# Kernel tuning notes

Hardware: AMD Instinct MI355X
Metric: run time of the kernel (lower is better)

Reference implementation:

```python
import jax, jax.numpy as jnp
import numpy as np
import math

B, S, IN_DIM, OUT_DIM = 16, 1024, 512, 256
THETA = 10000.0


def _rope_single(x, cos, sin):
    # x: [B,S,D]; cos/sin: [D//2] -- SAME rotation applied at every position
    # (faithful to original: freqs_cis[seq_len*2] selects a single row)
    xr = x.reshape(x.shape[0], x.shape[1], -1, 2)
    a, b = xr[..., 0], xr[..., 1]
    out = jnp.stack([a * cos - b * sin, a * sin + b * cos], axis=-1)
    return out.reshape(x.shape)


def setup_inputs() -> dict:
    key = jax.random.key(0)
    ks = jax.random.split(key, 4)
    scale = 1.0 / math.sqrt(IN_DIM)
    x = jax.random.normal(ks[0], (B, S, IN_DIM), jnp.float32)
    wq = jax.random.normal(ks[1], (OUT_DIM, IN_DIM), jnp.float32) * scale
    wk = jax.random.normal(ks[2], (OUT_DIM, IN_DIM), jnp.float32) * scale
    wv = jax.random.normal(ks[3], (OUT_DIM, IN_DIM), jnp.float32) * scale
    bq = jnp.zeros((OUT_DIM,), jnp.float32)
    bk = jnp.zeros((OUT_DIM,), jnp.float32)
    bv = jnp.zeros((OUT_DIM,), jnp.float32)
    return {"x": x, "wq": wq, "bq": bq, "wk": wk, "bk": bk, "wv": wv, "bv": bv}


def reference(x, wq, bq, wk, bk, wv, bv):
    dim = x.shape[-1]  # scale uses INPUT dim, per original code
    # freqs_cis row at position index = 2*seq_len
    inv_freq = 1.0 / (THETA ** (jnp.arange(0, OUT_DIM, 2, dtype=jnp.float32) / OUT_DIM))
    angle = (2.0 * S) * inv_freq  # [OUT_DIM//2]
    cos, sin = jnp.cos(angle), jnp.sin(angle)

    q = jnp.einsum('bsi,oi->bso', x, wq) + bq
    k = jnp.einsum('bsi,oi->bso', x, wk) + bk
    v = jnp.einsum('bsi,oi->bso', x, wv) + bv

    q = _rope_single(q, cos, sin)
    k = _rope_single(k, cos, sin)

    scores = jnp.einsum('bqd,bkd->bqk', q, k) / jnp.sqrt(jnp.float32(dim))
    scores = jax.nn.softmax(scores.astype(jnp.float32), axis=-1)
    out = jnp.einsum('bqk,bkd->bqd', scores, v)
    return out
```

## Files before the change

kernel.cpp:

```cpp
#include <hip/hip_runtime.h>
#include <hip/hip_bf16.h>


typedef __attribute__((ext_vector_type(8))) short short8;
typedef __attribute__((ext_vector_type(4))) short short4v;
typedef __attribute__((ext_vector_type(4))) float f32x4;

#define GLL16(g, l)                                                            \
  __builtin_amdgcn_global_load_lds(                                            \
      (const __attribute__((address_space(1))) unsigned int*)(g),              \
      (__attribute__((address_space(3))) unsigned int*)(l), 16, 0, 0)

static __device__ __forceinline__ short f2bf(float f) {
  __hip_bfloat16 h = __float2bfloat16(f);
  return __builtin_bit_cast(short, h);
}

__global__ void cvt_w(const float* __restrict__ wq, const float* __restrict__ wk,
                      const float* __restrict__ wv, short* __restrict__ dst) {
  int i = blockIdx.x * blockDim.x + threadIdx.x;
  if (i >= 49152) return;
  const float* src;
  int off;
  if (i < 16384)      { src = wq; off = i; }
  else if (i < 32768) { src = wk; off = i - 16384; }
  else                { src = wv; off = i - 32768; }
  const float4* sp = reinterpret_cast<const float4*>(src) + off * 2;
  float4 a = sp[0], b = sp[1];
  short8 o;
  o[0] = f2bf(a.x); o[1] = f2bf(a.y); o[2] = f2bf(a.z); o[3] = f2bf(a.w);
  o[4] = f2bf(b.x); o[5] = f2bf(b.y); o[6] = f2bf(b.z); o[7] = f2bf(b.w);
  *(reinterpret_cast<short8*>(dst) + i) = o;
}

__global__ __launch_bounds__(256) void qkv_gemm(
    const float* __restrict__ x, const short* __restrict__ wb,
    const float* __restrict__ bq, const float* __restrict__ bk,
    const float* __restrict__ bv, short* __restrict__ qb,
    short* __restrict__ kb, short* __restrict__ vt) {
  __shared__ __align__(16) char smem[32768];
  const int bid = blockIdx.x;
  const int swz = (bid & 7) * 96 + (bid >> 3);
  const int mt = swz / 6, nt = swz % 6;
  const int tid = threadIdx.x;
  const int w = tid >> 6, lane = tid & 63;
  const int g = lane >> 4, c = lane & 15;
  const int wm = w >> 1, wn = w & 1;

  f32x4 acc[4][4];
  const f32x4 fzero = {0.f, 0.f, 0.f, 0.f};
#pragma unroll
  for (int mi = 0; mi < 4; mi++)
#pragma unroll
    for (int ni = 0; ni < 4; ni++) acc[mi][ni] = fzero;

  const int arow = tid >> 4;
  const int acol4 = tid & 15;
  const int achunk = acol4 >> 1, ahalf = (tid & 1) * 8;

  for (int kk = 0; kk < 8; ++kk) {
    __syncthreads();
#pragma unroll
    for (int i = 0; i < 4; i++) {
      int idx = w * 4 + i;
      int r = idx * 8 + (lane >> 3);
      int cc = lane & 7;
      GLL16(wb + (nt * 128 + r) * 512 + kk * 64 + ((cc ^ (r & 7)) * 8),
            smem + 16384 + idx * 1024);
    }
    float4 xv[8];
#pragma unroll
    for (int j = 0; j < 8; j++) {
      int row = j * 16 + arow;
      xv[j] = *(const float4*)(x + (mt * 128 + row) * 512 + kk * 64 + acol4 * 4);
    }
#pragma unroll
    for (int j = 0; j < 8; j++) {
      int row = j * 16 + arow;
      short4v s4;
      s4[0] = f2bf(xv[j].x); s4[1] = f2bf(xv[j].y);
      s4[2] = f2bf(xv[j].z); s4[3] = f2bf(xv[j].w);
      *(short4v*)(smem + row * 128 + ((achunk ^ (row & 7)) * 16) + ahalf) = s4;
    }
    asm volatile("s_waitcnt vmcnt(0)" ::: "memory");
    __syncthreads();
#pragma unroll
    for (int ks = 0; ks < 2; ++ks) {
      short8 af[4], bf[4];
#pragma unroll
      for (int mi = 0; mi < 4; mi++) {
        int row = wm * 64 + mi * 16 + c;
        af[mi] = *(const short8*)(smem + row * 128 + (((ks * 4 + g) ^ (row & 7)) * 16));
      }
#pragma unroll
      for (int ni = 0; ni < 4; ni++) {
        int row = wn * 64 + ni * 16 + c;
        bf[ni] = *(const short8*)(smem + 16384 + row * 128 + (((ks * 4 + g) ^ (row & 7)) * 16));
      }
#pragma unroll
      for (int mi = 0; mi < 4; mi++)
#pragma unroll
        for (int ni = 0; ni < 4; ni++)
          acc[mi][ni] = __builtin_amdgcn_mfma_f32_16x16x32_bf16(af[mi], bf[ni], acc[mi][ni], 0, 0, 0);
    }
  }

  const int colbase = nt * 128 + wn * 64;
  const int cls = colbase >> 8;
  const int cw = colbase & 255;
  const int rowbase = mt * 128 + wm * 64;
  if (cls == 0) {
#pragma unroll
    for (int ni = 0; ni < 4; ni++) {
      int col = cw + ni * 16 + c;
      float bias = bq[col];
#pragma unroll
      for (int mi = 0; mi < 4; mi++)
#pragma unroll
        for (int j = 0; j < 4; j++) {
          int row = rowbase + mi * 16 + g * 4 + j;
          qb[row * 256 + col] = f2bf((acc[mi][ni][j] + bias) * 0.044194173824159216f);
        }
    }
  } else if (cls == 1) {
#pragma unroll
    for (int ni = 0; ni < 4; ni++) {
      int col = cw + ni * 16 + c;
      float bias = bk[col];
#pragma unroll
      for (int mi = 0; mi < 4; mi++)
#pragma unroll
        for (int j = 0; j < 4; j++) {
          int row = rowbase + mi * 16 + g * 4 + j;
          kb[row * 256 + col] = f2bf(acc[mi][ni][j] + bias);
        }
    }
  } else {
    __syncthreads();
    char* tb = smem + w * 8192;
#pragma unroll
    for (int ni = 0; ni < 4; ni++) {
      int dl = ni * 16 + c;
      float bias = bv[cw + dl];
#pragma unroll
      for (int mi = 0; mi < 4; mi++)
#pragma unroll
        for (int j = 0; j < 4; j++) {
          int sl = mi * 16 + g * 4 + j;
          *(short*)(tb + dl * 128 + ((sl * 2) ^ ((dl & 7) << 4))) =
              f2bf(acc[mi][ni][j] + bias);
        }
    }
    const int bb = rowbase >> 10, sb = rowbase & 1023;
#pragma unroll
    for (int i = 0; i < 8; i++) {
      int dl = i * 8 + (lane >> 3);
      int ch = lane & 7;
      short8 val = *(const short8*)(tb + dl * 128 + (((ch ^ (dl & 7)) * 16)));
      *(short8*)(vt + (bb * 256 + cw + dl) * 1024 + sb + ch * 8) = val;
    }
  }
}

__global__ __launch_bounds__(256) void attn_kernel(
    const short* __restrict__ qb, const short* __restrict__ kb,
    const short* __restrict__ vt, float* __restrict__ out) {
  __shared__ __align__(16) char smem[140288];
  const int bid = blockIdx.x;
  const int swz = (bid & 7) * 32 + (bid >> 3);
  const int b = swz >> 4, qt = swz & 15;
  const int tid = threadIdx.x;
  const int w = tid >> 6, lane = tid & 63;
  const int g = lane >> 4, c = lane & 15;
  const int q0 = b * 1024 + qt * 64 + w * 16;
  const int VB = 65536, PB = 131072;
  short* sp = (short*)(smem + PB + w * 2304);

  short8 qf[8];
#pragma unroll
  for (int ks = 0; ks < 8; ks++)
    qf[ks] = *(const short8*)(qb + (q0 + c) * 256 + ks * 32 + g * 8);

  f32x4 O[16];
  const f32x4 fzero = {0.f, 0.f, 0.f, 0.f};
#pragma unroll
  for (int ni = 0; ni < 16; ni++) O[ni] = fzero;
  float m_[4] = {-1e30f, -1e30f, -1e30f, -1e30f};
  float l_[4] = {0.f, 0.f, 0.f, 0.f};

  auto stage = [&](int kt, int bsel) {
    if (w < 2) {
#pragma unroll
      for (int i = 0; i < 16; i++) {
        int j = w * 16 + i;
        int r = j * 2 + (lane >> 5);
        int cc = lane & 31;
        GLL16(kb + (b * 1024 + kt * 64 + r) * 256 + ((cc ^ (r & 7)) * 8),
              smem + bsel * 32768 + j * 1024);
      }
    } else {
#pragma unroll
      for (int i = 0; i < 16; i++) {
        int j = (w - 2) * 16 + i;
        int r = j * 8 + (lane >> 3);
        int cc = lane & 7;
        GLL16(vt + (b * 256 + r) * 1024 + kt * 64 + ((cc ^ (r & 7)) * 8),
              smem + VB + bsel * 32768 + j * 1024);
      }
    }
  };

  stage(0, 0);
  for (int kt = 0; kt < 16; ++kt) {
    const int cur = kt & 1;
    const char* kbase = smem + cur * 32768;
    const char* vbase = smem + VB + cur * 32768;
    asm volatile("s_waitcnt vmcnt(0)" ::: "memory");
    __syncthreads();
    if (kt < 15) stage(kt + 1, cur ^ 1);

    f32x4 Sf[4];
#pragma unroll
    for (int nf = 0; nf < 4; nf++) Sf[nf] = fzero;
#pragma unroll
    for (int ks = 0; ks < 8; ks++) {
      short8 kf[4];
#pragma unroll
      for (int nf = 0; nf < 4; nf++) {
        int key = nf * 16 + c;
        kf[nf] = *(const short8*)(kbase + key * 512 + (((ks * 4 + g) ^ (c & 7)) * 16));
      }
#pragma unroll
      for (int nf = 0; nf < 4; nf++)
        Sf[nf] = __builtin_amdgcn_mfma_f32_16x16x32_bf16(qf[ks], kf[nf], Sf[nf], 0, 0, 0);
    }

    float Pv[4][4], scl[4];
#pragma unroll
    for (int j = 0; j < 4; j++) {
      float tm = fmaxf(fmaxf(Sf[0][j], Sf[1][j]), fmaxf(Sf[2][j], Sf[3][j]));
      tm = fmaxf(tm, __shfl_xor(tm, 1));
      tm = fmaxf(tm, __shfl_xor(tm, 2));
      tm = fmaxf(tm, __shfl_xor(tm, 4));
      tm = fmaxf(tm, __shfl_xor(tm, 8));
      float nm = fmaxf(m_[j], tm);
      scl[j] = __expf(m_[j] - nm);
      m_[j] = nm;
      float rs = 0.f;
#pragma unroll
      for (int nf = 0; nf < 4; nf++) {
        float p = __expf(Sf[nf][j] - nm);
        Pv[nf][j] = p;
        rs += p;
      }
      rs += __shfl_xor(rs, 1);
      rs += __shfl_xor(rs, 2);
      rs += __shfl_xor(rs, 4);
      rs += __shfl_xor(rs, 8);
      l_[j] = l_[j] * scl[j] + rs;
    }
#pragma unroll
    for (int ni = 0; ni < 16; ni++) {
      O[ni][0] *= scl[0]; O[ni][1] *= scl[1];
      O[ni][2] *= scl[2]; O[ni][3] *= scl[3];
    }

#pragma unroll
    for (int nf = 0; nf < 4; nf++)
#pragma unroll
      for (int j = 0; j < 4; j++)
        sp[(g * 4 + j) * 72 + nf * 16 + c] = f2bf(Pv[nf][j]);

    short8 pf[2];
#pragma unroll
    for (int ks2 = 0; ks2 < 2; ks2++)
      pf[ks2] = *(const short8*)((char*)sp + c * 144 + ks2 * 64 + g * 16);

#pragma unroll
    for (int ni = 0; ni < 16; ni++) {
      int d = ni * 16 + c;
#pragma unroll
      for (int ks2 = 0; ks2 < 2; ks2++) {
        short8 vf = *(const short8*)(vbase + d * 128 + (((ks2 * 4 + g) ^ (c & 7)) * 16));
        O[ni] = __builtin_amdgcn_mfma_f32_16x16x32_bf16(pf[ks2], vf, O[ni], 0, 0, 0);
      }
    }
  }

#pragma unroll
  for (int j = 0; j < 4; j++) {
    float inv = 1.0f / l_[j];
    int row = q0 + g * 4 + j;
#pragma unroll
    for (int ni = 0; ni < 16; ni++)
      out[row * 256 + ni * 16 + c] = O[ni][j] * inv;
  }
}

extern "C" void kernel_launch(void* const* d_in, const int* in_sizes, int n_in,
                              void* d_out, int out_size, void* d_ws, size_t ws_size,
                              hipStream_t stream) {
  const float* x  = (const float*)d_in[0];
  const float* wq = (const float*)d_in[1];
  const float* bq = (const float*)d_in[2];
  const float* wk = (const float*)d_in[3];
  const float* bk = (const float*)d_in[4];
  const float* wv = (const float*)d_in[5];
  const float* bv = (const float*)d_in[6];
  float* out = (float*)d_out;
  char* ws = (char*)d_ws;
  short* wb = (short*)ws;
  short* qb = (short*)(ws + 786432);
  short* kb = (short*)(ws + 9175040);
  short* vt = (short*)(ws + 17563648);

  cvt_w<<<192, 256, 0, stream>>>(wq, wk, wv, wb);
  qkv_gemm<<<768, 256, 0, stream>>>(x, wb, bq, bk, bv, qb, kb, vt);
  attn_kernel<<<256, 256, 0, stream>>>(qb, kb, vt, out);
}
```

Before: 167.0 us.

## Fuse weight conversion into QKV GEMM and split attention keys across two wave groups

Drops the separate weight-conversion kernel. The QKV GEMM now loads fp32 weights directly and converts them to bf16 while staging them into shared memory, which removes one launch and the extra weight round trip. The attention kernel moves to 512 threads: two groups of four waves each process half of the key sequence, and their partial softmax states are merged through shared memory at the end (split-K flash attention). The key/value double-buffer prefetch is dropped in favour of synchronous loads per tile, so load latency may be less hidden, and the larger block may lower occupancy.

```diff
diff --git a/kernel.cpp b/kernel.cpp
--- a/kernel.cpp
+++ b/kernel.cpp
@@ -16,25 +16,9 @@
   return __builtin_bit_cast(short, h);
 }
 
-__global__ void cvt_w(const float* __restrict__ wq, const float* __restrict__ wk,
-                      const float* __restrict__ wv, short* __restrict__ dst) {
-  int i = blockIdx.x * blockDim.x + threadIdx.x;
-  if (i >= 49152) return;
-  const float* src;
-  int off;
-  if (i < 16384)      { src = wq; off = i; }
-  else if (i < 32768) { src = wk; off = i - 16384; }
-  else                { src = wv; off = i - 32768; }
-  const float4* sp = reinterpret_cast<const float4*>(src) + off * 2;
-  float4 a = sp[0], b = sp[1];
-  short8 o;
-  o[0] = f2bf(a.x); o[1] = f2bf(a.y); o[2] = f2bf(a.z); o[3] = f2bf(a.w);
-  o[4] = f2bf(b.x); o[5] = f2bf(b.y); o[6] = f2bf(b.z); o[7] = f2bf(b.w);
-  *(reinterpret_cast<short8*>(dst) + i) = o;
-}
-
 __global__ __launch_bounds__(256) void qkv_gemm(
-    const float* __restrict__ x, const short* __restrict__ wb,
+    const float* __restrict__ x, const float* __restrict__ wq,
+    const float* __restrict__ wk, const float* __restrict__ wv,
     const float* __restrict__ bq, const float* __restrict__ bk,
     const float* __restrict__ bv, short* __restrict__ qb,
     short* __restrict__ kb, short* __restrict__ vt) {
@@ -47,6 +31,9 @@
   const int g = lane >> 4, c = lane & 15;
   const int wm = w >> 1, wn = w & 1;
 
+  const float* wsel = (nt < 2) ? wq : (nt < 4) ? wk : wv;
+  const int wro = (nt & 1) * 128;
+
   f32x4 acc[4][4];
   const f32x4 fzero = {0.f, 0.f, 0.f, 0.f};
 #pragma unroll
@@ -60,19 +47,16 @@
 
   for (int kk = 0; kk < 8; ++kk) {
     __syncthreads();
-#pragma unroll
-    for (int i = 0; i < 4; i++) {
-      int idx = w * 4 + i;
-      int r = idx * 8 + (lane >> 3);
-      int cc = lane & 7;
-      GLL16(wb + (nt * 128 + r) * 512 + kk * 64 + ((cc ^ (r & 7)) * 8),
-            smem + 16384 + idx * 1024);
-    }
-    float4 xv[8];
+    float4 xv[8], wv8[8];
 #pragma unroll
     for (int j = 0; j < 8; j++) {
       int row = j * 16 + arow;
       xv[j] = *(const float4*)(x + (mt * 128 + row) * 512 + kk * 64 + acol4 * 4);
+    }
+#pragma unroll
+    for (int j = 0; j < 8; j++) {
+      int row = j * 16 + arow;
+      wv8[j] = *(const float4*)(wsel + (wro + row) * 512 + kk * 64 + acol4 * 4);
     }
 #pragma unroll
     for (int j = 0; j < 8; j++) {
@@ -81,8 +65,11 @@
       s4[0] = f2bf(xv[j].x); s4[1] = f2bf(xv[j].y);
       s4[2] = f2bf(xv[j].z); s4[3] = f2bf(xv[j].w);
       *(short4v*)(smem + row * 128 + ((achunk ^ (row & 7)) * 16) + ahalf) = s4;
-    }
-    asm volatile("s_waitcnt vmcnt(0)" ::: "memory");
+      short4v t4;
+      t4[0] = f2bf(wv8[j].x); t4[1] = f2bf(wv8[j].y);
+      t4[2] = f2bf(wv8[j].z); t4[3] = f2bf(wv8[j].w);
+      *(short4v*)(smem + 16384 + row * 128 + ((achunk ^ (row & 7)) * 16) + ahalf) = t4;
+    }
     __syncthreads();
 #pragma unroll
     for (int ks = 0; ks < 2; ++ks) {
@@ -105,9 +92,8 @@
     }
   }
 
-  const int colbase = nt * 128 + wn * 64;
-  const int cls = colbase >> 8;
-  const int cw = colbase & 255;
+  const int cls = nt >> 1;
+  const int cw = (nt & 1) * 128 + wn * 64;
   const int rowbase = mt * 128 + wm * 64;
   if (cls == 0) {
 #pragma unroll
@@ -156,25 +142,27 @@
     for (int i = 0; i < 8; i++) {
       int dl = i * 8 + (lane >> 3);
       int ch = lane & 7;
-      short8 val = *(const short8*)(tb + dl * 128 + (((ch ^ (dl & 7)) * 16)));
+      short8 val = *(const short8*)(tb + dl * 128 + ((ch ^ (dl & 7)) * 16));
       *(short8*)(vt + (bb * 256 + cw + dl) * 1024 + sb + ch * 8) = val;
     }
   }
 }
 
-__global__ __launch_bounds__(256) void attn_kernel(
+__global__ __launch_bounds__(512) void attn_kernel(
     const short* __restrict__ qb, const short* __restrict__ kb,
     const short* __restrict__ vt, float* __restrict__ out) {
-  __shared__ __align__(16) char smem[140288];
+  __shared__ __align__(16) char smem[149504];
   const int bid = blockIdx.x;
   const int swz = (bid & 7) * 32 + (bid >> 3);
   const int b = swz >> 4, qt = swz & 15;
   const int tid = threadIdx.x;
   const int w = tid >> 6, lane = tid & 63;
+  const int grp = w >> 2, lw = w & 3;
   const int g = lane >> 4, c = lane & 15;
-  const int q0 = b * 1024 + qt * 64 + w * 16;
-  const int VB = 65536, PB = 131072;
-  short* sp = (short*)(smem + PB + w * 2304);
+  const int q0 = b * 1024 + qt * 64 + lw * 16;
+  char* kbase = smem + grp * 32768;
+  char* vbase = smem + 65536 + grp * 32768;
+  short* sp = (short*)(smem + 131072 + w * 2304);
 
   short8 qf[8];
 #pragma unroll
@@ -188,36 +176,31 @@
   float m_[4] = {-1e30f, -1e30f, -1e30f, -1e30f};
   float l_[4] = {0.f, 0.f, 0.f, 0.f};
 
-  auto stage = [&](int kt, int bsel) {
-    if (w < 2) {
+  const int krow0 = b * 1024 + grp * 512;
+
+  for (int kt = 0; kt < 8; ++kt) {
+    __syncthreads();
+    if (lw < 2) {
 #pragma unroll
       for (int i = 0; i < 16; i++) {
-        int j = w * 16 + i;
+        int j = lw * 16 + i;
         int r = j * 2 + (lane >> 5);
         int cc = lane & 31;
-        GLL16(kb + (b * 1024 + kt * 64 + r) * 256 + ((cc ^ (r & 7)) * 8),
-              smem + bsel * 32768 + j * 1024);
+        GLL16(kb + (krow0 + kt * 64 + r) * 256 + ((cc ^ (r & 7)) * 8),
+              kbase + j * 1024);
       }
     } else {
 #pragma unroll
       for (int i = 0; i < 16; i++) {
-        int j = (w - 2) * 16 + i;
+        int j = (lw - 2) * 16 + i;
         int r = j * 8 + (lane >> 3);
         int cc = lane & 7;
-        GLL16(vt + (b * 256 + r) * 1024 + kt * 64 + ((cc ^ (r & 7)) * 8),
-              smem + VB + bsel * 32768 + j * 1024);
-      }
-    }
-  };
-
-  stage(0, 0);
-  for (int kt = 0; kt < 16; ++kt) {
-    const int cur = kt & 1;
-    const char* kbase = smem + cur * 32768;
-    const char* vbase = smem + VB + cur * 32768;
+        GLL16(vt + (b * 256 + r) * 1024 + grp * 512 + kt * 64 + ((cc ^ (r & 7)) * 8),
+              vbase + j * 1024);
+      }
+    }
     asm volatile("s_waitcnt vmcnt(0)" ::: "memory");
     __syncthreads();
-    if (kt < 15) stage(kt + 1, cur ^ 1);
 
     f32x4 Sf[4];
 #pragma unroll
@@ -287,13 +270,42 @@
     }
   }
 
-#pragma unroll
-  for (int j = 0; j < 4; j++) {
-    float inv = 1.0f / l_[j];
-    int row = q0 + g * 4 + j;
+  __syncthreads();
+  if (grp == 1) {
+    char* ob = smem + lw * 20480;
 #pragma unroll
     for (int ni = 0; ni < 16; ni++)
-      out[row * 256 + ni * 16 + c] = O[ni][j] * inv;
+      *(f32x4*)(ob + (ni * 16 + c) * 80 + g * 16) = O[ni];
+    float2* mlb = (float2*)(smem + 131072);
+#pragma unroll
+    for (int j = 0; j < 4; j++) {
+      float2 ml; ml.x = m_[j]; ml.y = l_[j];
+      mlb[lw * 16 + g * 4 + j] = ml;
+    }
+  }
+  __syncthreads();
+  if (grp == 0) {
+    char* ob = smem + lw * 20480;
+    const float2* mlb = (const float2*)(smem + 131072);
+    float a1[4], a2[4], inv[4];
+#pragma unroll
+    for (int j = 0; j < 4; j++) {
+      float2 ml2 = mlb[lw * 16 + g * 4 + j];
+      float mm = fmaxf(m_[j], ml2.x);
+      a1[j] = __expf(m_[j] - mm);
+      a2[j] = __expf(ml2.x - mm);
+      float l = a1[j] * l_[j] + a2[j] * ml2.y;
+      inv[j] = 1.0f / l;
+    }
+#pragma unroll
+    for (int ni = 0; ni < 16; ni++) {
+      f32x4 o2 = *(const f32x4*)(ob + (ni * 16 + c) * 80 + g * 16);
+#pragma unroll
+      for (int j = 0; j < 4; j++) {
+        int row = q0 + g * 4 + j;
+        out[row * 256 + ni * 16 + c] = (a1[j] * O[ni][j] + a2[j] * o2[j]) * inv[j];
+      }
+    }
   }
 }
 
@@ -309,12 +321,10 @@
   const float* bv = (const float*)d_in[6];
   float* out = (float*)d_out;
   char* ws = (char*)d_ws;
-  short* wb = (short*)ws;
-  short* qb = (short*)(ws + 786432);
-  short* kb = (short*)(ws + 9175040);
-  short* vt = (short*)(ws + 17563648);
-
-  cvt_w<<<192, 256, 0, stream>>>(wq, wk, wv, wb);
-  qkv_gemm<<<768, 256, 0, stream>>>(x, wb, bq, bk, bv, qb, kb, vt);
-  attn_kernel<<<256, 256, 0, stream>>>(qb, kb, vt, out);
+  short* qb = (short*)ws;
+  short* kb = (short*)(ws + 8388608);
+  short* vt = (short*)(ws + 16777216);
+
+  qkv_gemm<<<768, 256, 0, stream>>>(x, wq, wk, wv, bq, bk, bv, qb, kb, vt);
+  attn_kernel<<<256, 512, 0, stream>>>(qb, kb, vt, out);
 }
```

New measurement: 156.3 us. -6.4%, faster.
